# Kernel optimization log

Measured on AMD Instinct MI355X. Metric: run time of the kernel, lower is better.

The kernel has to match this reference:

```python
import jax, jax.numpy as jnp
import numpy as np

B = 256
WIN = 20          # input image side; 20 -> 12 -> 4 so num_routes = 32*4*4 = 512
ROUTES = 512
NCAPS = 10
DOUT = 16
DIN = 8
REC = 256 * WIN * WIN  # 102400


def _conv(x, w):
    return jax.lax.conv_general_dilated(x, w, (1, 1), 'VALID',
                                        dimension_numbers=('NCHW', 'OIHW', 'NCHW'))


def setup_inputs() -> dict:
    key = jax.random.key(0)
    ks = jax.random.split(key, 12)
    n = lambda k, shape, sc: (jax.random.normal(k, shape, jnp.float32) * sc)
    return {
        'data':    jax.random.normal(ks[0], (B, 1, WIN, WIN), jnp.float32),
        'conv1_w': n(ks[1], (256, 1, 9, 9), 0.1),
        'conv1_b': jnp.zeros((256,), jnp.float32),
        'prim_w':  n(ks[2], (8 * 32, 256, 9, 9), 0.007),  # 8 capsule convs fused: [8*32,256,9,9]
        'prim_b':  jnp.zeros((8 * 32,), jnp.float32),
        'W_digit': n(ks[3], (ROUTES, NCAPS, DOUT, DIN), 0.05),
        'dec_w1':  n(ks[4], (512, NCAPS * DOUT), 0.05),
        'dec_b1':  jnp.zeros((512,), jnp.float32),
        'dec_w2':  n(ks[5], (1024, 512), 0.04),
        'dec_b2':  jnp.zeros((1024,), jnp.float32),
        'dec_w3':  n(ks[6], (REC, 1024), 0.03),
        'dec_b3':  jnp.zeros((REC,), jnp.float32),
    }


def reference(data, conv1_w, conv1_b, prim_w, prim_b, W_digit,
              dec_w1, dec_b1, dec_w2, dec_b2, dec_w3, dec_b3):
    Bn = data.shape[0]
    # ConvLayer: 9x9 VALID conv + relu -> [B,256,12,12]
    h = jax.nn.relu(_conv(data, conv1_w) + conv1_b[None, :, None, None])
    # PrimaryCaps: 8 parallel convs (fused as one 256-out conv) -> [B,8,32,4,4]
    u = _conv(h, prim_w) + prim_b[None, :, None, None]
    H, W = u.shape[2], u.shape[3]
    u = u.reshape(Bn, 8, 32, H, W)
    # torch's u.view(B, 32*H*W, -1): raw row-major reshape of (8,32,H,W) -> (32*H*W, 8)
    u = u.reshape(Bn, 32 * H * W, 8)
    # vector squash over last (8-dim) axis
    sn = jnp.sum(u * u, axis=-1, keepdims=True)
    x = sn * u / ((1.0 + sn) * jnp.sqrt(sn))          # [B,R,8]
    # DigitCaps: u_hat[b,r,c,o] = W[r,c,o,i] x[b,r,i]
    u_hat = jnp.einsum('rcoi,bri->brco', W_digit, x)  # [B,R,10,16]
    b_ij = jnp.zeros((ROUTES, NCAPS), u_hat.dtype)    # shared over batch, as in original
    v = None
    for it in range(3):
        c = jax.nn.softmax(b_ij, axis=0)              # softmax over routes
        s = jnp.einsum('rc,brco->bco', c, u_hat)      # [B,10,16]
        # NOTE: original squash sums over a trailing dim of size 1 -> elementwise squash
        sq = s * s
        v = sq * s / ((1.0 + sq) * jnp.sqrt(sq))      # [B,10,16]
        if it < 2:
            a = jnp.einsum('brco,bco->brc', u_hat, v)
            b_ij = b_ij + jnp.mean(a, axis=0)
    # Decoder
    classes = jnp.sqrt(jnp.sum(v * v, axis=2))        # [B,10]
    classes = jax.nn.softmax(classes, axis=0)         # legacy F.softmax on 3D -> dim 0
    idx = jnp.argmax(classes, axis=1)                 # [B]
    masked = jax.nn.one_hot(idx, NCAPS, dtype=v.dtype)
    flat = (v * masked[:, :, None]).reshape(Bn, -1)   # [B,160]
    h1 = jax.nn.relu(flat @ dec_w1.T + dec_b1)
    h2 = jax.nn.relu(h1 @ dec_w2.T + dec_b2)
    rec = jax.nn.sigmoid(h2 @ dec_w3.T + dec_b3)
    return rec.reshape(-1, 256, WIN, WIN)
```

## Files before the change

### kernel.cpp

```cpp
#include <hip/hip_runtime.h>
#include <cmath>


constexpr int BATCH = 256;

enum { AM_PLAIN = 0, AM_CONV1 = 1 };
enum { EPI_NONE = 0, EPI_RELU = 1, EPI_SIG = 2, EPI_RELU_SPLIT = 3, EPI_RELU_H2B = 4 };

typedef short bf16x8 __attribute__((ext_vector_type(8)));
typedef unsigned short us8 __attribute__((ext_vector_type(8)));
typedef float f32x4 __attribute__((ext_vector_type(4)));

__device__ __forceinline__ unsigned short f2b(float v) {
  unsigned int u = __float_as_uint(v);
  u += 0x7FFFu + ((u >> 16) & 1u);
  return (unsigned short)(u >> 16);
}
__device__ __forceinline__ void split_bf(float v, unsigned short& h, unsigned short& l) {
  h = f2b(v);
  l = f2b(v - __uint_as_float(((unsigned int)h) << 16));
}

template <int BM, int BN, int TM, int TN, int AMODE, int EPI>
__global__ __launch_bounds__(256, 2) void gemm_k(
    const float* __restrict__ A, const float* __restrict__ Bm,
    const float* __restrict__ bias, float* __restrict__ C,
    int M, int N, int K, int k_len,
    unsigned short* __restrict__ Chi, unsigned short* __restrict__ Clo) {
  static_assert(TM == 8 && TN == 8, "microtile fixed at 8x8");
  constexpr int BK = 8;
  constexpr int TX = BN / TN;

  const int tid = threadIdx.x;
  const int tx = tid % TX;
  const int ty = tid / TX;
  const int n0 = blockIdx.x * BN;
  const int m0 = blockIdx.y * BM;
  const int k_begin = blockIdx.z * k_len;
  const int k_end = k_begin + k_len;
  C += (size_t)blockIdx.z * (size_t)M * (size_t)N;

  __shared__ float As[BK][BM + 4];
  __shared__ float Bs[BK][BN + 4];

  float acc[TM][TN] = {};

  for (int kt = k_begin; kt < k_end; kt += BK) {
    __syncthreads();
    for (int base = tid * 4; base < BM * BK; base += 1024) {
      int ml = base / BK;
      int kl = base % BK;
#pragma unroll
      for (int j = 0; j < 4; j++) {
        int k = kt + kl + j;
        float v = 0.f;
        if (k < k_end) {
          if constexpr (AMODE == AM_PLAIN) {
            v = A[(size_t)(m0 + ml) * K + k];
          } else {
            int m = m0 + ml;
            int b = m / 144, p = m - b * 144;
            int py = p / 12, px = p - py * 12;
            int ky = k / 9, kx = k - ky * 9;
            v = A[b * 400 + (py + ky) * 20 + (px + kx)];
          }
        }
        As[kl + j][ml] = v;
      }
    }
    for (int base = tid * 4; base < BN * BK; base += 1024) {
      int nl = base / BK;
      int kl = base % BK;
#pragma unroll
      for (int j = 0; j < 4; j++) {
        int k = kt + kl + j;
        float v = 0.f;
        if (k < k_end) v = Bm[(size_t)(n0 + nl) * K + k];
        Bs[kl + j][nl] = v;
      }
    }
    __syncthreads();
#pragma unroll
    for (int kk = 0; kk < BK; kk++) {
      float af[TM], bf[TN];
      const float4* ap = reinterpret_cast<const float4*>(&As[kk][ty * TM]);
      reinterpret_cast<float4*>(af)[0] = ap[0];
      reinterpret_cast<float4*>(af)[1] = ap[1];
      const float4* bp = reinterpret_cast<const float4*>(&Bs[kk][tx * TN]);
      reinterpret_cast<float4*>(bf)[0] = bp[0];
      reinterpret_cast<float4*>(bf)[1] = bp[1];
#pragma unroll
      for (int i = 0; i < TM; i++)
#pragma unroll
        for (int j = 0; j < TN; j++) acc[i][j] += af[i] * bf[j];
    }
  }

#pragma unroll
  for (int i = 0; i < TM; i++) {
    int m = m0 + ty * TM + i;
#pragma unroll
    for (int j = 0; j < TN; j++) {
      int n = n0 + tx * TN + j;
      float v = acc[i][j];
      if constexpr (EPI == EPI_RELU) {
        v += bias[n];
        v = fmaxf(v, 0.f);
        C[(size_t)m * N + n] = v;
      } else if constexpr (EPI == EPI_SIG) {
        v += bias[n];
        v = 1.f / (1.f + expf(-v));
        C[(size_t)m * N + n] = v;
      } else if constexpr (EPI == EPI_RELU_SPLIT) {
        v += bias[n];
        v = fmaxf(v, 0.f);
        unsigned short hs, ls;
        split_bf(v, hs, ls);
        Chi[(size_t)m * N + n] = hs;
        Clo[(size_t)m * N + n] = ls;
      } else if constexpr (EPI == EPI_RELU_H2B) {
        v += bias[n];
        v = fmaxf(v, 0.f);
        Chi[(size_t)m * N + n] = f2b(v);
      } else {
        C[(size_t)m * N + n] = v;
      }
    }
  }
}

__global__ void transpose_w_k(const float* __restrict__ w,
                              unsigned short* __restrict__ hi,
                              unsigned short* __restrict__ lo) {
  int idx = blockIdx.x * 256 + threadIdx.x;
  if (idx >= 256 * 20736) return;
  int n = idx / 20736;
  int rem = idx - n * 20736;
  int kk = rem >> 8;
  int cin = rem & 255;
  float v = w[n * 20736 + cin * 81 + kk];
  unsigned short h, l;
  split_bf(v, h, l);
  hi[idx] = h;
  lo[idx] = l;
}

__global__ __launch_bounds__(256, 2) void prim_mfma_k(
    const unsigned short* __restrict__ Ahi, const unsigned short* __restrict__ Alo,
    const unsigned short* __restrict__ Bhi, const unsigned short* __restrict__ Blo,
    float* __restrict__ part) {
  __shared__ unsigned short Ah[128 * 64], Al[128 * 64];
  __shared__ unsigned short Bh[128 * 64], Bl[128 * 64];

  const int tid = threadIdx.x;
  const int wave = tid >> 6, lane = tid & 63;
  const int wm = (wave >> 1) * 64, wn = (wave & 1) * 64;
  const int cl = lane & 15, rq = lane >> 4;
  const int n0 = blockIdx.x * 128;
  const int m0 = blockIdx.y * 128;
  const int z = blockIdx.z;
  const int k_begin = z * 1728, k_end = k_begin + 1728;

  f32x4 acc[4][4];
#pragma unroll
  for (int i = 0; i < 4; i++)
#pragma unroll
    for (int j = 0; j < 4; j++) acc[i][j] = f32x4{0.f, 0.f, 0.f, 0.f};

  for (int kt = k_begin; kt < k_end; kt += 64) {
    const int kk = kt >> 8;
    const int cin0 = kt & 255;
    const int dy = kk / 9, dx = kk - dy * 9;
    __syncthreads();
#pragma unroll
    for (int j = 0; j < 4; j++) {
      int g = j * 256 + tid;
      int row = g >> 3, c = g & 7;
      int ld = row * 64 + ((c ^ (row & 7)) << 3);
      int m = m0 + row;
      int b = m >> 4, q = m & 15;
      int y = q >> 2, xx = q & 3;
      size_t ga = ((size_t)(b * 144 + (y + dy) * 12 + (xx + dx)) << 8) + cin0 + c * 8;
      *(us8*)&Ah[ld] = *(const us8*)(Ahi + ga);
      *(us8*)&Al[ld] = *(const us8*)(Alo + ga);
      size_t gb = (size_t)(n0 + row) * 20736 + kt + c * 8;
      *(us8*)&Bh[ld] = *(const us8*)(Bhi + gb);
      *(us8*)&Bl[ld] = *(const us8*)(Blo + gb);
    }
    __syncthreads();

#pragma unroll
    for (int ko = 0; ko < 64; ko += 32) {
      const int cb = ko >> 3;
      bf16x8 a_hi[4], b_hi[4], t[4];
#pragma unroll
      for (int im = 0; im < 4; im++) {
        int r = wm + im * 16 + cl;
        a_hi[im] = *(const bf16x8*)&Ah[r * 64 + (((cb + rq) ^ (cl & 7)) << 3)];
      }
#pragma unroll
      for (int in = 0; in < 4; in++) {
        int r = wn + in * 16 + cl;
        b_hi[in] = *(const bf16x8*)&Bh[r * 64 + (((cb + rq) ^ (cl & 7)) << 3)];
      }
#pragma unroll
      for (int im = 0; im < 4; im++)
#pragma unroll
        for (int in = 0; in < 4; in++)
          acc[im][in] = __builtin_amdgcn_mfma_f32_16x16x32_bf16(a_hi[im], b_hi[in],
                                                                acc[im][in], 0, 0, 0);
#pragma unroll
      for (int in = 0; in < 4; in++) {
        int r = wn + in * 16 + cl;
        t[in] = *(const bf16x8*)&Bl[r * 64 + (((cb + rq) ^ (cl & 7)) << 3)];
      }
#pragma unroll
      for (int im = 0; im < 4; im++)
#pragma unroll
        for (int in = 0; in < 4; in++)
          acc[im][in] = __builtin_amdgcn_mfma_f32_16x16x32_bf16(a_hi[im], t[in],
                                                                acc[im][in], 0, 0, 0);
#pragma unroll
      for (int im = 0; im < 4; im++) {
        int r = wm + im * 16 + cl;
        t[im] = *(const bf16x8*)&Al[r * 64 + (((cb + rq) ^ (cl & 7)) << 3)];
      }
#pragma unroll
      for (int im = 0; im < 4; im++)
#pragma unroll
        for (int in = 0; in < 4; in++)
          acc[im][in] = __builtin_amdgcn_mfma_f32_16x16x32_bf16(t[im], b_hi[in],
                                                                acc[im][in], 0, 0, 0);
    }
  }

  float* Cp = part + (size_t)z * 1048576;
#pragma unroll
  for (int in = 0; in < 4; in++) {
    int n = n0 + wn + in * 16 + cl;
#pragma unroll
    for (int im = 0; im < 4; im++)
#pragma unroll
      for (int r = 0; r < 4; r++) {
        int m = m0 + wm + im * 16 + rq * 4 + r;
        Cp[(size_t)m * 256 + n] = acc[im][in][r];
      }
  }
}

__global__ __launch_bounds__(256, 2) void dec3_mfma_k(
    const unsigned short* __restrict__ Ab,
    const float* __restrict__ Bw,
    const float* __restrict__ bias,
    float* __restrict__ C) {
  constexpr int K = 1024, N = 102400;
  __shared__ unsigned short As[256 * 64];
  __shared__ unsigned short Bs[64 * 64];

  const int tid = threadIdx.x;
  const int wave = tid >> 6, lane = tid & 63;
  const int cl = lane & 15, rq = lane >> 4;
  const int n0 = blockIdx.x * 64;

  f32x4 acc[4][4];
#pragma unroll
  for (int i = 0; i < 4; i++)
#pragma unroll
    for (int j = 0; j < 4; j++) acc[i][j] = f32x4{0.f, 0.f, 0.f, 0.f};

  for (int kt = 0; kt < K; kt += 64) {
    __syncthreads();
#pragma unroll
    for (int j = 0; j < 8; j++) {
      int g = j * 256 + tid;
      int row = g >> 3, c = g & 7;
      int ld = row * 64 + ((c ^ (row & 7)) << 3);
      *(us8*)&As[ld] = *(const us8*)(Ab + (size_t)row * K + kt + c * 8);
    }
#pragma unroll
    for (int j = 0; j < 2; j++) {
      int g = j * 256 + tid;
      int row = g >> 3, c = g & 7;
      int ld = row * 64 + ((c ^ (row & 7)) << 3);
      const float* src = Bw + (size_t)(n0 + row) * K + kt + c * 8;
      float4 v0 = *(const float4*)src;
      float4 v1 = *(const float4*)(src + 4);
      us8 h;
      h[0] = f2b(v0.x); h[1] = f2b(v0.y); h[2] = f2b(v0.z); h[3] = f2b(v0.w);
      h[4] = f2b(v1.x); h[5] = f2b(v1.y); h[6] = f2b(v1.z); h[7] = f2b(v1.w);
      *(us8*)&Bs[ld] = h;
    }
    __syncthreads();
#pragma unroll
    for (int ko = 0; ko < 64; ko += 32) {
      const int cb = ko >> 3;
      bf16x8 af[4], bq[4];
#pragma unroll
      for (int im = 0; im < 4; im++) {
        int r = wave * 64 + im * 16 + cl;
        af[im] = *(const bf16x8*)&As[r * 64 + (((cb + rq) ^ (cl & 7)) << 3)];
      }
#pragma unroll
      for (int in = 0; in < 4; in++) {
        int r = in * 16 + cl;
        bq[in] = *(const bf16x8*)&Bs[r * 64 + (((cb + rq) ^ (cl & 7)) << 3)];
      }
#pragma unroll
      for (int im = 0; im < 4; im++)
#pragma unroll
        for (int in = 0; in < 4; in++)
          acc[im][in] = __builtin_amdgcn_mfma_f32_16x16x32_bf16(af[im], bq[in],
                                                                acc[im][in], 0, 0, 0);
    }
  }

#pragma unroll
  for (int in = 0; in < 4; in++) {
    int n = n0 + in * 16 + cl;
    float bn = bias[n];
#pragma unroll
    for (int im = 0; im < 4; im++)
#pragma unroll
      for (int r = 0; r < 4; r++) {
        int m = wave * 64 + im * 16 + rq * 4 + r;
        float v = acc[im][in][r] + bn;
        v = 1.f / (1.f + expf(-v));
        C[(size_t)m * N + n] = v;
      }
  }
}

__global__ void red_squash_k(const float* __restrict__ part,
                             const float* __restrict__ prim_b,
                             float* __restrict__ x) {
  const int chg = blockIdx.x;
  const int b = blockIdx.y;
  const int tid = threadIdx.x;
  const int ch_l = tid & 15;
  const int q = tid >> 4;
  const int ch = chg * 16 + ch_l;

  float val = prim_b[ch];
#pragma unroll
  for (int z = 0; z < 12; z++) val += part[z * 1048576 + (b * 16 + q) * 256 + ch];

  __shared__ float su[16][17];
  su[q][ch_l] = val;
  __syncthreads();

  const int vec = tid >> 3;
  const int i = tid & 7;
  const int ch_l2 = vec >> 1;
  const int t = vec & 1;
  float sn = 0.f;
#pragma unroll
  for (int ii = 0; ii < 8; ii++) {
    float e = su[8 * t + ii][ch_l2];
    sn += e * e;
  }
  float factor = sn / ((1.f + sn) * sqrtf(sn));
  float e = su[8 * t + i][ch_l2];
  int chh = chg * 16 + ch_l2;
  int d8 = chh >> 5, d32 = chh & 31;
  int r = d8 * 64 + d32 * 2 + t;
  x[b * 4096 + r * 8 + i] = e * factor;
}

__global__ void uhat_k(const float* __restrict__ W, const float* __restrict__ x,
                       float* __restrict__ uhat) {
  const int r = blockIdx.x;
  const int tid = threadIdx.x;
  __shared__ float Wl[8 * 160];
  __shared__ float xl[256 * 8];
  for (int t = tid; t < 1280; t += 256) {
    int co = t >> 3, i = t & 7;
    Wl[i * 160 + co] = W[r * 1280 + t];
  }
  for (int t = tid; t < 2048; t += 256) {
    int b = t >> 3, i = t & 7;
    xl[t] = x[b * 4096 + r * 8 + i];
  }
  __syncthreads();
  for (int item = tid; item < 256 * 160; item += 256) {
    int b = item / 160;
    int co = item - b * 160;
    float acc = 0.f;
#pragma unroll
    for (int i = 0; i < 8; i++) acc += Wl[i * 160 + co] * xl[b * 8 + i];
    uhat[b * 81920 + r * 160 + co] = acc;
  }
}

__global__ void zero_b_k(float* __restrict__ bij) {
  int id = blockIdx.x * 256 + threadIdx.x;
  if (id < 5120) bij[id] = 0.f;
}

__global__ void route_iter_k(const float* __restrict__ uhat,
                             const float* __restrict__ c_rc,
                             float* __restrict__ v_out,
                             float* __restrict__ a_buf,
                             int use_uniform, int do_update) {
  const int b = blockIdx.x;
  const int tid = threadIdx.x;
  __shared__ float c_l[5120];
  __shared__ float v_l[160];
  if (!use_uniform) {
    for (int t = tid; t < 5120; t += 256) c_l[t] = c_rc[t];
  }
  __syncthreads();
  if (tid < 160) {
    const float* up = uhat + b * 81920 + tid;
    const int cls = tid >> 4;
    float acc = 0.f;
    if (use_uniform) {
#pragma unroll 8
      for (int r = 0; r < 512; r++) acc += up[r * 160];
      acc *= (1.f / 512.f);
    } else {
#pragma unroll 8
      for (int r = 0; r < 512; r++) acc += c_l[r * 10 + cls] * up[r * 160];
    }
    float sq = acc * acc;
    float vv = sq * acc / ((1.f + sq) * sqrtf(sq));
    v_l[tid] = vv;
    v_out[b * 160 + tid] = vv;
  }
  __syncthreads();
  if (do_update) {
    for (int item = tid; item < 5120; item += 256) {
      int r = item / 10;
      int c = item - r * 10;
      const float* up2 = uhat + b * 81920 + r * 160 + c * 16;
      float a = 0.f;
#pragma unroll
      for (int o = 0; o < 16; o++) a += up2[o] * v_l[c * 16 + o];
      a_buf[b * 5120 + item] = a;
    }
  }
}

__global__ void bupd_k(const float* __restrict__ a_buf, float* __restrict__ bij) {
  int id = blockIdx.x * 256 + threadIdx.x;
  if (id >= 5120) return;
  float s = 0.f;
  for (int b = 0; b < BATCH; b++) s += a_buf[b * 5120 + id];
  bij[id] += s * (1.f / 256.f);
}

__global__ void softmax_b_k(const float* __restrict__ bij, float* __restrict__ c_rc) {
  const int tid = threadIdx.x;
  __shared__ float Ml[10], Sl[10];
  if (tid < 10) {
    float m = -1e30f;
    for (int r = 0; r < 512; r++) m = fmaxf(m, bij[r * 10 + tid]);
    float s = 0.f;
    for (int r = 0; r < 512; r++) s += expf(bij[r * 10 + tid] - m);
    Ml[tid] = m;
    Sl[tid] = s;
  }
  __syncthreads();
  if (tid < 512) {
    for (int c = 0; c < 10; c++)
      c_rc[tid * 10 + c] = expf(bij[tid * 10 + c] - Ml[c]) / Sl[c];
  }
}

__global__ void classes_k(const float* __restrict__ v, float* __restrict__ sel,
                          int* __restrict__ idxb) {
  const int b = threadIdx.x;
  float cl[10], ex[10];
  for (int c = 0; c < 10; c++) {
    float s = 0.f;
    for (int o = 0; o < 16; o++) {
      float e = v[b * 160 + c * 16 + o];
      s += e * e;
    }
    cl[c] = sqrtf(s);
  }
  __shared__ float red[256];
  __shared__ float Mc[10], Sc[10];
  for (int c = 0; c < 10; c++) {
    red[b] = cl[c];
    __syncthreads();
    for (int s = 128; s > 0; s >>= 1) {
      if (b < s) red[b] = fmaxf(red[b], red[b + s]);
      __syncthreads();
    }
    if (b == 0) Mc[c] = red[0];
    __syncthreads();
  }
  for (int c = 0; c < 10; c++) {
    ex[c] = expf(cl[c] - Mc[c]);
    red[b] = ex[c];
    __syncthreads();
    for (int s = 128; s > 0; s >>= 1) {
      if (b < s) red[b] += red[b + s];
      __syncthreads();
    }
    if (b == 0) Sc[c] = red[0];
    __syncthreads();
  }
  float best = ex[0] / Sc[0];
  int bi = 0;
  for (int c = 1; c < 10; c++) {
    float p = ex[c] / Sc[c];
    if (p > best) { best = p; bi = c; }
  }
  idxb[b] = bi;
  for (int o = 0; o < 16; o++) sel[b * 16 + o] = v[b * 160 + bi * 16 + o];
}

__global__ void h1_k(const float* __restrict__ sel, const int* __restrict__ idxb,
                     const float* __restrict__ w1, const float* __restrict__ b1,
                     float* __restrict__ h1) {
  const int b = blockIdx.x;
  const int j = threadIdx.x;
  __shared__ float ssel[16];
  __shared__ int six;
  if (j < 16) ssel[j] = sel[b * 16 + j];
  if (j == 0) six = idxb[b];
  __syncthreads();
  const float* wrow = w1 + j * 160 + six * 16;
  float acc = b1[j];
#pragma unroll
  for (int o = 0; o < 16; o++) acc += ssel[o] * wrow[o];
  h1[b * 512 + j] = fmaxf(acc, 0.f);
}

extern "C" void kernel_launch(void* const* d_in, const int* in_sizes, int n_in,
                              void* d_out, int out_size, void* d_ws, size_t ws_size,
                              hipStream_t stream) {
  const float* data    = (const float*)d_in[0];
  const float* conv1_w = (const float*)d_in[1];
  const float* conv1_b = (const float*)d_in[2];
  const float* prim_w  = (const float*)d_in[3];
  const float* prim_b  = (const float*)d_in[4];
  const float* W_digit = (const float*)d_in[5];
  const float* dec_w1  = (const float*)d_in[6];
  const float* dec_b1  = (const float*)d_in[7];
  const float* dec_w2  = (const float*)d_in[8];
  const float* dec_b2  = (const float*)d_in[9];
  const float* dec_w3  = (const float*)d_in[10];
  const float* dec_b3  = (const float*)d_in[11];
  float* out = (float*)d_out;

  float* ws = (float*)d_ws;
  float* uhat = ws;
  float* part = ws;
  unsigned short* h_hi  = (unsigned short*)(ws + 20971520);
  unsigned short* h_lo  = (unsigned short*)(ws + 25690112);
  unsigned short* wT_hi = (unsigned short*)(ws + 30408704);
  unsigned short* wT_lo = (unsigned short*)(ws + 33062912);
  float* x    = ws + 20971520;
  float* v    = ws + 22020096;
  float* bij  = ws + 22061056;
  float* crc  = ws + 22066176;
  float* abuf = ws + 22071296;
  float* sel  = ws + 23382016;
  int*   idxb = (int*)(ws + 23386112);
  float* h1   = ws + 23386368;
  unsigned short* h2b = (unsigned short*)(ws + 23517440);
  float* dummyC = ws + 23648512;

  transpose_w_k<<<20736, 256, 0, stream>>>(prim_w, wT_hi, wT_lo);

  gemm_k<128, 128, 8, 8, AM_CONV1, EPI_RELU_SPLIT>
      <<<dim3(2, 288, 1), 256, 0, stream>>>(data, conv1_w, conv1_b, nullptr,
                                            36864, 256, 81, 81, h_hi, h_lo);

  prim_mfma_k<<<dim3(2, 32, 12), 256, 0, stream>>>(h_hi, h_lo, wT_hi, wT_lo, part);

  red_squash_k<<<dim3(16, 256), 256, 0, stream>>>(part, prim_b, x);

  uhat_k<<<512, 256, 0, stream>>>(W_digit, x, uhat);

  zero_b_k<<<20, 256, 0, stream>>>(bij);
  route_iter_k<<<256, 256, 0, stream>>>(uhat, crc, v, abuf, 1, 1);
  bupd_k<<<20, 256, 0, stream>>>(abuf, bij);
  softmax_b_k<<<1, 512, 0, stream>>>(bij, crc);
  route_iter_k<<<256, 256, 0, stream>>>(uhat, crc, v, abuf, 0, 1);
  bupd_k<<<20, 256, 0, stream>>>(abuf, bij);
  softmax_b_k<<<1, 512, 0, stream>>>(bij, crc);
  route_iter_k<<<256, 256, 0, stream>>>(uhat, crc, v, nullptr, 0, 0);

  classes_k<<<1, 256, 0, stream>>>(v, sel, idxb);

  h1_k<<<256, 512, 0, stream>>>(sel, idxb, dec_w1, dec_b1, h1);
  gemm_k<128, 128, 8, 8, AM_PLAIN, EPI_RELU_H2B>
      <<<dim3(8, 2, 1), 256, 0, stream>>>(h1, dec_w2, dec_b2, dummyC,
                                          256, 1024, 512, 512, h2b, nullptr);
  dec3_mfma_k<<<dim3(1600, 1, 1), 256, 0, stream>>>(h2b, dec_w3, dec_b3, out);
}
```

Before: 1.336 ms.

## Stage weight transpose through LDS and use direct global-to-LDS loads in prim GEMM

The weight transpose/split kernel now reads each output channel's half contiguously into shared memory, using a skewed layout, and writes the transposed rows out coalesced, instead of doing a strided gather per element. The primary-caps MFMA kernel replaces register-staged global-to-LDS copies with global_load_lds 16-byte direct loads, with per-thread address components precomputed outside the K loop. This is meant to cut uncoalesced memory traffic and VGPR/instruction overhead in the tile loads. It relies on the LDS destination pattern matching the wave-contiguous layout that global_load_lds requires, and the swizzle is now applied on the source side.

```diff
diff --git a/kernel.cpp b/kernel.cpp
--- a/kernel.cpp
+++ b/kernel.cpp
@@ -19,6 +19,12 @@
 __device__ __forceinline__ void split_bf(float v, unsigned short& h, unsigned short& l) {
   h = f2b(v);
   l = f2b(v - __uint_as_float(((unsigned int)h) << 16));
+}
+
+__device__ __forceinline__ void gload16(unsigned short* lds, const unsigned short* g) {
+  __builtin_amdgcn_global_load_lds(
+      (const __attribute__((address_space(1))) unsigned int*)(g),
+      (__attribute__((address_space(3))) unsigned int*)(lds), 16, 0, 0);
 }
 
 template <int BM, int BN, int TM, int TN, int AMODE, int EPI>
@@ -132,17 +138,29 @@
 __global__ void transpose_w_k(const float* __restrict__ w,
                               unsigned short* __restrict__ hi,
                               unsigned short* __restrict__ lo) {
-  int idx = blockIdx.x * 256 + threadIdx.x;
-  if (idx >= 256 * 20736) return;
-  int n = idx / 20736;
-  int rem = idx - n * 20736;
-  int kk = rem >> 8;
-  int cin = rem & 255;
-  float v = w[n * 20736 + cin * 81 + kk];
-  unsigned short h, l;
-  split_bf(v, h, l);
-  hi[idx] = h;
-  lo[idx] = l;
+  __shared__ unsigned short shi[10368], slo[10368];
+  const int n = blockIdx.x >> 1;
+  const int h = blockIdx.x & 1;
+  const int tid = threadIdx.x;
+  const float* src = w + n * 20736 + h * 10368;
+  for (int i = tid; i < 10368; i += 256) {
+    float v = src[i];
+    int cin_l = i / 81, kk = i - cin_l * 81;
+    int idx = kk * 128 + ((cin_l + 2 * kk) & 127);
+    unsigned short hb, lb;
+    split_bf(v, hb, lb);
+    shi[idx] = hb;
+    slo[idx] = lb;
+  }
+  __syncthreads();
+  unsigned short* dh = hi + n * 20736 + h * 128;
+  unsigned short* dl = lo + n * 20736 + h * 128;
+  for (int j = tid; j < 10368; j += 256) {
+    int kk = j >> 7, cin_l = j & 127;
+    int idx = (j & ~127) + ((cin_l + 2 * kk) & 127);
+    dh[kk * 256 + cin_l] = shi[idx];
+    dl[kk * 256 + cin_l] = slo[idx];
+  }
 }
 
 __global__ __launch_bounds__(256, 2) void prim_mfma_k(
@@ -161,6 +179,24 @@
   const int z = blockIdx.z;
   const int k_begin = z * 1728, k_end = k_begin + 1728;
 
+  int s_ldso[4];
+  int s_arow[4];
+  int s_cp8[4];
+  size_t s_gb[4];
+#pragma unroll
+  for (int t = 0; t < 4; t++) {
+    int g = (wave * 4 + t) * 64 + lane;
+    int row = g >> 3, c = g & 7;
+    int cp = c ^ (row & 7);
+    s_ldso[t] = (wave * 4 + t) * 512;
+    s_cp8[t] = cp * 8;
+    int m = m0 + row;
+    int b = m >> 4, q = m & 15;
+    int y = q >> 2, xx = q & 3;
+    s_arow[t] = b * 144 + y * 12 + xx;
+    s_gb[t] = (size_t)(n0 + row) * 20736 + cp * 8;
+  }
+
   f32x4 acc[4][4];
 #pragma unroll
   for (int i = 0; i < 4; i++)
@@ -171,21 +207,16 @@
     const int kk = kt >> 8;
     const int cin0 = kt & 255;
     const int dy = kk / 9, dx = kk - dy * 9;
-    __syncthreads();
-#pragma unroll
-    for (int j = 0; j < 4; j++) {
-      int g = j * 256 + tid;
-      int row = g >> 3, c = g & 7;
-      int ld = row * 64 + ((c ^ (row & 7)) << 3);
-      int m = m0 + row;
-      int b = m >> 4, q = m & 15;
-      int y = q >> 2, xx = q & 3;
-      size_t ga = ((size_t)(b * 144 + (y + dy) * 12 + (xx + dx)) << 8) + cin0 + c * 8;
-      *(us8*)&Ah[ld] = *(const us8*)(Ahi + ga);
-      *(us8*)&Al[ld] = *(const us8*)(Alo + ga);
-      size_t gb = (size_t)(n0 + row) * 20736 + kt + c * 8;
-      *(us8*)&Bh[ld] = *(const us8*)(Bhi + gb);
-      *(us8*)&Bl[ld] = *(const us8*)(Blo + gb);
+    const int dyx = dy * 12 + dx;
+    __syncthreads();
+#pragma unroll
+    for (int t = 0; t < 4; t++) {
+      size_t ga = ((size_t)(s_arow[t] + dyx) << 8) + cin0 + s_cp8[t];
+      size_t gb = s_gb[t] + kt;
+      gload16(&Ah[s_ldso[t]], Ahi + ga);
+      gload16(&Al[s_ldso[t]], Alo + ga);
+      gload16(&Bh[s_ldso[t]], Bhi + gb);
+      gload16(&Bl[s_ldso[t]], Blo + gb);
     }
     __syncthreads();
 
@@ -563,7 +594,7 @@
   unsigned short* h2b = (unsigned short*)(ws + 23517440);
   float* dummyC = ws + 23648512;
 
-  transpose_w_k<<<20736, 256, 0, stream>>>(prim_w, wT_hi, wT_lo);
+  transpose_w_k<<<512, 256, 0, stream>>>(prim_w, wT_hi, wT_lo);
 
   gemm_k<128, 128, 8, 8, AM_CONV1, EPI_RELU_SPLIT>
       <<<dim3(2, 288, 1), 256, 0, stream>>>(data, conv1_w, conv1_b, nullptr,
```

After: 1.329 ms. No clear change (-0.5%).
